# Optimization experiments

Measured on AMD Instinct MI355X. Metric: run time of the kernel, lower is better.

The kernel has to match this reference:

```python
import jax, jax.numpy as jnp
import numpy as np

H = 16        # num heads
ALPHA = 1.3   # entmax alpha
N_ITER = 50   # bisection iterations
EPS = 1e-5    # layernorm eps


def entmax_bisect(x, alpha=ALPHA, n_iter=N_ITER):
    # x: (..., K). Bisection entmax along last axis (Peters et al. 2019).
    am1 = alpha - 1.0
    x = x - jnp.max(x, axis=-1, keepdims=True)
    m = jnp.max(x, axis=-1, keepdims=True)  # == 0 after shift
    lo, hi = m - 10.0, m + 10.0
    def step(carry, _):
        lo, hi = carry
        mid = 0.5 * (lo + hi)
        p = jnp.maximum(am1 * x - mid, 0.0) ** (1.0 / am1)
        gt = jnp.sum(p, axis=-1, keepdims=True) > 1.0
        return (jnp.where(gt, mid, lo), jnp.where(gt, hi, mid)), None
    (lo, hi), _ = jax.lax.scan(jax.checkpoint(step), (lo, hi), None, length=n_iter)
    p = jnp.maximum(am1 * x - hi, 0.0) ** (1.0 / am1)
    return p / (jnp.sum(p, axis=-1, keepdims=True) + 1e-12)


def _heads(t, B, N, hd):
    return t.reshape(B, N, H, hd).transpose(0, 2, 1, 3)  # (B,H,N,hd)


def attn_branch(x, mask, wq, bq, wk, bk, wv, bv, wo, bo, use_entmax):
    B, N, D = x.shape
    hd = D // H
    q = _heads(x @ wq + bq, B, N, hd)
    k = _heads(x @ wk + bk, B, N, hd)
    v = _heads(x @ wv + bv, B, N, hd)
    s = jnp.einsum('bhqd,bhkd->bhqk', q, k) / float(np.sqrt(hd)) + mask
    if use_entmax:
        s = s - jnp.max(s, axis=-1, keepdims=True)
        a = entmax_bisect(s)
    else:
        a = jax.nn.softmax(s, axis=-1)
    o = jnp.einsum('bhqk,bhkd->bhqd', a, v).transpose(0, 2, 1, 3).reshape(B, N, D)
    return o @ wo + bo


def layer_norm(x, g, b):
    m = jnp.mean(x, axis=-1, keepdims=True)
    v = jnp.mean((x - m) ** 2, axis=-1, keepdims=True)
    return (x - m) * jax.lax.rsqrt(v + EPS) * g + b


def setup_inputs():
    B, N, D, F, FILM, NMODS = 4, 512, 2048, 8192, 64, 10000
    key = jax.random.key(0)
    ks = iter(jax.random.split(key, 64))
    rn = lambda *s: jax.random.normal(next(ks), s, dtype=jnp.float32)
    inp = dict(
        x=rn(B, N, D),
        attn_mask_intra=jnp.zeros((N, N), jnp.float32),
        attn_mask_inter=jnp.zeros((N, N), jnp.float32),
        mods=jax.random.randint(next(ks), (B, N), 0, 9999),
        film_emb=rn(NMODS, FILM) * 0.02,
        film_gw=rn(FILM, D) * 0.02, film_gb=jnp.zeros((D,), jnp.float32),
        film_bw=rn(FILM, D) * 0.02, film_bb=jnp.zeros((D,), jnp.float32),
        gate_alpha=jnp.zeros((2,), jnp.float32),
        ln1_g=jnp.ones((D,), jnp.float32), ln1_b=jnp.zeros((D,), jnp.float32),
        ln2_g=jnp.ones((D,), jnp.float32), ln2_b=jnp.zeros((D,), jnp.float32),
        ffn_w1=rn(D, F) * 0.02, ffn_b1=jnp.zeros((F,), jnp.float32),
        ffn_w2=rn(F, D) * 0.02, ffn_b2=jnp.zeros((D,), jnp.float32),
    )
    for tag in ('a', 'e'):
        for nm in ('q', 'k', 'v', 'o'):
            inp['w%s_%s' % (nm, tag)] = rn(D, D) * 0.02
            inp['b%s_%s' % (nm, tag)] = jnp.zeros((D,), jnp.float32)
    return inp


def reference(x, attn_mask_intra, attn_mask_inter, mods,
              film_emb, film_gw, film_gb, film_bw, film_bb,
              gate_alpha, ln1_g, ln1_b, ln2_g, ln2_b,
              ffn_w1, ffn_b1, ffn_w2, ffn_b2,
              wq_a, bq_a, wk_a, bk_a, wv_a, bv_a, wo_a, bo_a,
              wq_e, bq_e, wk_e, bk_e, wv_e, bv_e, wo_e, bo_e):
    # FiLM modulation on the intra-module branch input
    e = film_emb[jnp.clip(mods, 1, None)]                      # (B,N,FILM)
    y_intra = (1.0 + e @ film_gw + film_gb) * x + (e @ film_bw + film_bb)
    z_intra = attn_branch(y_intra, attn_mask_intra, wq_a, bq_a, wk_a, bk_a,
                          wv_a, bv_a, wo_a, bo_a, use_entmax=False)
    z_inter = attn_branch(x, attn_mask_inter, wq_e, bq_e, wk_e, bk_e,
                          wv_e, bv_e, wo_e, bo_e, use_entmax=True)
    w = jax.nn.softmax(gate_alpha)                              # global gate
    z = w[0] * z_intra + w[1] * z_inter
    h = layer_norm(x + z, ln1_g, ln1_b)                         # Post-LN
    y = jax.nn.relu(h @ ffn_w1 + ffn_b1) @ ffn_w2 + ffn_b2
    return layer_norm(h + y, ln2_g, ln2_b)
```

## Files before the change

### kernel.cpp

```cpp
#include <hip/hip_runtime.h>
#include <hip/hip_bf16.h>

typedef float f32x4 __attribute__((ext_vector_type(4)));
typedef short bf16x8 __attribute__((ext_vector_type(8)));
typedef unsigned short u16;

#define SEQ    512
#define DIM    2048
#define NHEAD  16
#define HDIM   128
#define BATCH  4
#define BTOK   2048
#define FFDIM  8192
#define DSZ    ((long)BTOK*DIM)
#define QKVN   (3*DIM)
#define QKVSZ  ((long)BTOK*QKVN)
#define ISS    0.08838834764831845f

__device__ __forceinline__ u16 f2bf(float f){
  union{float fv;unsigned u;}c;c.fv=f;
  unsigned r=c.u+0x7FFFu+((c.u>>16)&1u); return (u16)(r>>16);
}
__device__ __forceinline__ float bf2f(u16 v){
  union{unsigned u;float f;}c;c.u=((unsigned)v)<<16;return c.f;
}
__device__ __forceinline__ float pow103(float t){
  return __builtin_amdgcn_exp2f(__builtin_amdgcn_logf(t)*(10.0f/3.0f));
}

#define GLD16(g,l) __builtin_amdgcn_global_load_lds( \
    (const __attribute__((address_space(1))) unsigned int*)(g), \
    (__attribute__((address_space(3))) unsigned int*)(l), 16, 0, 0)

#define MF(a,b,c) __builtin_amdgcn_mfma_f32_16x16x32_bf16(a,b,c,0,0,0)
#define VMW(n) do{ asm volatile("s_waitcnt vmcnt(" #n ")" ::: "memory"); \
                   __builtin_amdgcn_sched_barrier(0); }while(0)
#define LGKM0() do{ asm volatile("s_waitcnt lgkmcnt(0)" ::: "memory"); \
                    __builtin_amdgcn_sched_barrier(0); }while(0)
#define BARR() do{ asm volatile("" ::: "memory"); __builtin_amdgcn_s_barrier(); \
                   asm volatile("" ::: "memory"); }while(0)

__global__ __launch_bounds__(256, 2)
void gemm4w(const u16* __restrict__ A, int lda, long sAo, long sAi,
            const u16* __restrict__ B, int ldb, long sBo, long sBi,
            u16* __restrict__ C, int ldc, long sCo,
            const float* __restrict__ bias, long sbias,
            int K, int hdiv, int relu)
{
  __shared__ __align__(16) u16 sm[36864];
  char* smb = (char*)sm;

  int gx = gridDim.x, gy = gridDim.y;
  int nwg = gx*gy*gridDim.z;
  int flat = (blockIdx.z*gy + blockIdx.y)*gx + blockIdx.x;
  int cpx = nwg >> 3; flat = (flat & 7)*cpx + (flat >> 3);
  int by = flat % gy; int tq = flat / gy; int bx = tq % gx; int bz = tq / gx;

  int zo = bz / hdiv, zi = bz - zo*hdiv;
  const u16* Ab = A + (long)zo*sAo + (long)zi*sAi;
  const u16* Bb = B + (long)zo*sBo + (long)zi*sBi;
  int m0 = by*128, n0 = bx*256;

  int tid = threadIdx.x, lane = tid & 63, w = tid >> 6;
  int lr = lane & 15, lg = lane >> 4;
  int rl = lane >> 2, cbyte = (lane & 3)*16;

  int sRA[2], sCA[2];
  #pragma unroll
  for (int q = 0; q < 2; q++) {
    int r = (2*w+q)*16 + rl;
    sRA[q] = r ^ ((r>>2)&1);
    sCA[q] = (cbyte ^ ((((r>>2)^r)&1)<<4) ^ (((r>>1)&1)<<5)) >> 1;
  }
  int sRB[4], sCB[4];
  #pragma unroll
  for (int q = 0; q < 4; q++) {
    int r = (4*w+q)*16 + rl;
    sRB[q] = r ^ ((r>>2)&1);
    sCB[q] = (cbyte ^ ((((r>>2)^r)&1)<<4) ^ (((r>>1)&1)<<5)) >> 1;
  }

  int aoff = (lr*64 + lg*16) ^ ((lane&7)<<4);
  int boff = w*4096 + ((lr*64 + lg*16) ^ ((lane&7)<<4));

  f32x4 acc[8][4] = {};
  int NT = K >> 5;

  auto STG = [&](int buf, int kt) {
    int kcol = kt*32;
    char* base = smb + buf*24576;
    #pragma unroll
    for (int q = 0; q < 2; q++)
      GLD16(Ab + (long)(m0 + sRA[q])*lda + kcol + sCA[q], base + (2*w+q)*1024);
    #pragma unroll
    for (int q = 0; q < 4; q++)
      GLD16(Bb + (long)(n0 + sRB[q])*ldb + kcol + sCB[q], base + 8192 + (4*w+q)*1024);
  };

  STG(0,0);
  if (NT > 1) STG(1,1);

  int buf = 0;
  for (int t = 0; t < NT; t++) {
    char* Ax = smb + buf*24576;
    char* Bx = Ax + 8192;

    if (t+2 < NT) {
      int nb = buf + 2; if (nb >= 3) nb -= 3;
      STG(nb, t+2);
      VMW(12);
    } else if (t+1 < NT) { VMW(6); }
    else                 { VMW(0); }
    BARR();

    bf16x8 af[8], bv[4];
    #pragma unroll
    for (int i = 0; i < 8; i++) af[i] = *(const bf16x8*)(Ax + aoff + i*1024);
    #pragma unroll
    for (int j = 0; j < 4; j++) bv[j] = *(const bf16x8*)(Bx + boff + j*1024);
    LGKM0();
    __builtin_amdgcn_s_setprio(1);
    #pragma unroll
    for (int i = 0; i < 8; i++) {
      acc[i][0] = MF(af[i], bv[0], acc[i][0]);
      acc[i][1] = MF(af[i], bv[1], acc[i][1]);
      acc[i][2] = MF(af[i], bv[2], acc[i][2]);
      acc[i][3] = MF(af[i], bv[3], acc[i][3]);
    }
    __builtin_amdgcn_s_setprio(0);
    BARR();
    buf++; if (buf == 3) buf = 0;
  }

  u16* Cb = C + (long)bz*sCo;
  #pragma unroll
  for (int j = 0; j < 4; j++) {
    int col = n0 + w*64 + j*16 + lr;
    float bv2 = bias ? bias[zo*sbias + col] : 0.0f;
    #pragma unroll
    for (int i = 0; i < 8; i++) {
      #pragma unroll
      for (int e = 0; e < 4; e++) {
        int row = m0 + i*16 + lg*4 + e;
        float v = acc[i][j][e] + bv2;
        if (relu) v = fmaxf(v, 0.0f);
        Cb[(long)row*ldc + col] = f2bf(v);
      }
    }
  }
}

__global__ __launch_bounds__(256, 3)
void gemm4(const u16* __restrict__ A, int lda, long sAo, long sAi,
           const u16* __restrict__ B, int ldb, long sBo, long sBi,
           void* __restrict__ C, int ldc, long sCo, long sCi, int outbf,
           const float* __restrict__ bias, long sbias,
           int K, int hdiv, int relu)
{
  __shared__ __align__(16) u16 sm[24576];
  char* smb = (char*)sm;

  int gx = gridDim.x, gy = gridDim.y;
  int nwg = gx*gy*gridDim.z;
  int flat = (blockIdx.z*gy + blockIdx.y)*gx + blockIdx.x;
  int cpx = nwg >> 3; flat = (flat & 7)*cpx + (flat >> 3);
  int by = flat % gy; int tq = flat / gy; int bx = tq % gx; int bz = tq / gx;

  int zo = bz / hdiv, zi = bz - zo*hdiv;
  const u16* Ab = A + (long)zo*sAo + (long)zi*sAi;
  const u16* Bb = B + (long)zo*sBo + (long)zi*sBi;
  int m0 = by*128, n0 = bx*128;

  int tid = threadIdx.x, lane = tid & 63, w = tid >> 6;
  int wrow = (w>>1)*64, wn = (w&1)*64;
  int lr = lane & 15, lg = lane >> 4;

  int stR[2], stC[2], ldsch[2];
  #pragma unroll
  for (int q = 0; q < 2; q++) {
    int chunk = q*4 + w;
    int r = chunk*16 + (lane>>2);
    int c = (lane&3)*16;
    int Rz = r ^ ((r>>2)&1);
    int Cz = c ^ ((((r>>2)^r)&1)<<4) ^ (((r>>1)&1)<<5);
    stR[q] = Rz; stC[q] = Cz>>1;
    ldsch[q] = chunk*1024;
  }

  int aoff = ((wrow + lr)*64 + lg*16) ^ ((lane&7)<<4);
  int boff = ((wn  + lr)*64 + lg*16) ^ ((lane&7)<<4);

  f32x4 acc[4][4] = {};
  int NT = K >> 5;

  auto STG = [&](int buf, int op, int kt) {
    const u16* gp = op ? Bb : Ab;
    int ld   = op ? ldb : lda;
    int base = op ? n0 : m0;
    int kcol = kt*32;
    #pragma unroll
    for (int q = 0; q < 2; q++) {
      const u16* src = gp + (long)(base + stR[q])*ld + kcol + stC[q];
      char* dst = smb + buf*16384 + op*8192 + ldsch[q];
      GLD16(src, dst);
    }
  };

  STG(0,0,0); STG(0,1,0);
  if (NT > 1) { STG(1,0,1); STG(1,1,1); }

  int buf = 0;
  for (int t = 0; t < NT; t++) {
    char* Ax = smb + buf*16384;
    char* Bx = smb + buf*16384 + 8192;

    if (t+2 < NT) {
      int nb = buf + 2; if (nb >= 3) nb -= 3;
      STG(nb,0,t+2); STG(nb,1,t+2);
      VMW(8);
    } else if (t+1 < NT) { VMW(4); }
    else                 { VMW(0); }
    BARR();

    bf16x8 af[4], bv[4];
    #pragma unroll
    for (int i = 0; i < 4; i++) af[i] = *(const bf16x8*)(Ax + aoff + i*1024);
    #pragma unroll
    for (int j = 0; j < 4; j++) bv[j] = *(const bf16x8*)(Bx + boff + j*1024);
    LGKM0();
    __builtin_amdgcn_s_setprio(1);
    #pragma unroll
    for (int i = 0; i < 4; i++) {
      acc[i][0] = MF(af[i], bv[0], acc[i][0]);
      acc[i][1] = MF(af[i], bv[1], acc[i][1]);
      acc[i][2] = MF(af[i], bv[2], acc[i][2]);
      acc[i][3] = MF(af[i], bv[3], acc[i][3]);
    }
    __builtin_amdgcn_s_setprio(0);
    BARR();
    buf++; if (buf == 3) buf = 0;
  }

  long coff = (long)zo*sCo + (long)zi*sCi;
  if (outbf) {
    u16* Cb = (u16*)C + coff;
    #pragma unroll
    for (int j = 0; j < 4; j++) {
      int col = n0 + wn + j*16 + lr;
      float bv2 = bias ? bias[zo*sbias + col] : 0.0f;
      #pragma unroll
      for (int i = 0; i < 4; i++) {
        #pragma unroll
        for (int e = 0; e < 4; e++) {
          int row = m0 + wrow + i*16 + lg*4 + e;
          float v = acc[i][j][e] + bv2;
          if (relu) v = fmaxf(v, 0.0f);
          Cb[(long)row*ldc + col] = f2bf(v);
        }
      }
    }
  } else {
    float* Cb = (float*)C + coff;
    #pragma unroll
    for (int j = 0; j < 4; j++) {
      int col = n0 + wn + j*16 + lr;
      #pragma unroll
      for (int i = 0; i < 4; i++) {
        #pragma unroll
        for (int e = 0; e < 4; e++) {
          int row = m0 + wrow + i*16 + lg*4 + e;
          Cb[(long)row*ldc + col] = acc[i][j][e];
        }
      }
    }
  }
}

__global__ __launch_bounds__(256, 2)
void qkprobs_both(const u16* __restrict__ QKVp,
                  const float* __restrict__ maskI, const float* __restrict__ maskE,
                  u16* __restrict__ Pall)
{
  __shared__ __align__(16) u16 sm[40960];
  char* smb = (char*)sm;

  int m0 = blockIdx.x*64;
  int z2 = blockIdx.y;
  int br = z2 >> 6, z = z2 & 63;
  int b  = z >> 4, h = z & 15;
  const float* maskp = br ? maskE : maskI;
  const u16* Qb = QKVp + (long)br*QKVSZ + (long)b*SEQ*QKVN + h*HDIM;
  const u16* Kb = Qb + DIM;
  u16* P = Pall + (long)br*64*SEQ*SEQ;

  int tid = threadIdx.x, lane = tid & 63, w = tid >> 6;
  int lr = lane & 15, lg = lane >> 4;
  int wn = w*128;

  int rl = lane >> 2;
  int cb = (lane & 3)*16;

  int aoff = (lr*64 + lg*16) ^ ((lane&7)<<4);
  int boff = ((wn + lr)*64 + lg*16) ^ ((lane&7)<<4);

  auto stgA = [&](int kt) {
    int r = w*16 + rl;
    int Rz = r ^ ((r>>2)&1);
    int Cz = cb ^ ((((r>>2)^r)&1)<<4) ^ (((r>>1)&1)<<5);
    GLD16(Qb + (long)(m0+Rz)*QKVN + kt*32 + (Cz>>1), smb + kt*4096 + w*1024);
  };
  auto stgB = [&](int buf, int kt) {
    #pragma unroll
    for (int q = 0; q < 8; q++) {
      int chunk = q*4 + w;
      int r = chunk*16 + rl;
      int Rz = r ^ ((r>>2)&1);
      int Cz = cb ^ ((((r>>2)^r)&1)<<4) ^ (((r>>1)&1)<<5);
      GLD16(Kb + (long)Rz*QKVN + kt*32 + (Cz>>1),
            smb + 16384 + buf*32768 + chunk*1024);
    }
  };

  f32x4 acc[4][8] = {};

  stgA(0); stgA(1); stgA(2); stgA(3);
  stgB(0,0);

  #pragma unroll
  for (int kt = 0; kt < 4; kt++) {
    if (kt < 3) { stgB((kt+1)&1, kt+1); VMW(8); } else { VMW(0); }
    BARR();
    char* Bx = smb + 16384 + (kt&1)*32768;
    bf16x8 af[4], bv[8];
    #pragma unroll
    for (int i = 0; i < 4; i++) af[i] = *(const bf16x8*)(smb + kt*4096 + aoff + i*1024);
    #pragma unroll
    for (int j = 0; j < 8; j++) bv[j] = *(const bf16x8*)(Bx + boff + j*1024);
    LGKM0();
    __builtin_amdgcn_s_setprio(1);
    #pragma unroll
    for (int i = 0; i < 4; i++)
      #pragma unroll
      for (int j = 0; j < 8; j++)
        acc[i][j] = MF(af[i], bv[j], acc[i][j]);
    __builtin_amdgcn_s_setprio(0);
    BARR();
  }

  float* redA = (float*)smb;
  float* redB = (float*)(smb + 1024);

  float rmax[16];
  #pragma unroll
  for (int s = 0; s < 16; s++) rmax[s] = -3.4e38f;
  #pragma unroll
  for (int i = 0; i < 4; i++) {
    #pragma unroll
    for (int e = 0; e < 4; e++) {
      int row = i*16 + lg*4 + e;
      const float* mp = maskp + (long)(m0+row)*SEQ + wn + lr;
      #pragma unroll
      for (int j = 0; j < 8; j++) {
        float v = acc[i][j][e]*ISS + mp[j*16];
        acc[i][j][e] = v;
        rmax[i*4+e] = fmaxf(rmax[i*4+e], v);
      }
    }
  }
  #pragma unroll
  for (int s = 0; s < 16; s++)
    #pragma unroll
    for (int o = 1; o < 16; o <<= 1) rmax[s] = fmaxf(rmax[s], __shfl_xor(rmax[s], o));
  if (lr == 0) {
    #pragma unroll
    for (int i = 0; i < 4; i++)
      #pragma unroll
      for (int e = 0; e < 4; e++) redA[w*64 + i*16 + lg*4 + e] = rmax[i*4+e];
  }
  BARR();
  #pragma unroll
  for (int i = 0; i < 4; i++)
    #pragma unroll
    for (int e = 0; e < 4; e++) {
      int row = i*16 + lg*4 + e;
      rmax[i*4+e] = fmaxf(fmaxf(redA[row], redA[64+row]),
                          fmaxf(redA[128+row], redA[192+row]));
    }
  BARR();

  float inv[16];

  if (br) {
    #pragma unroll
    for (int i = 0; i < 4; i++)
      #pragma unroll
      for (int j = 0; j < 8; j++)
        #pragma unroll
        for (int e = 0; e < 4; e++)
          acc[i][j][e] = (acc[i][j][e] - rmax[i*4+e])*0.3f;

    float lo[16], hi[16], tau[16];
    #pragma unroll
    for (int s = 0; s < 16; s++) { lo[s] = -1.0f; hi[s] = 0.0f; }

    #pragma unroll 1
    for (int it = 0; it < 5; it++) {
      float ps[16];
      #pragma unroll
      for (int s = 0; s < 16; s++) ps[s] = 0.0f;
      #pragma unroll
      for (int i = 0; i < 4; i++)
        #pragma unroll
        for (int e = 0; e < 4; e++) {
          float mid = 0.5f*(lo[i*4+e] + hi[i*4+e]);
          #pragma unroll
          for (int j = 0; j < 8; j++) {
            float t = acc[i][j][e] - mid;
            if (t > 0.0f) ps[i*4+e] += pow103(t);
          }
        }
      #pragma unroll
      for (int s = 0; s < 16; s++)
        #pragma unroll
        for (int o = 1; o < 16; o <<= 1) ps[s] += __shfl_xor(ps[s], o);
      if (lr == 0) {
        #pragma unroll
        for (int i = 0; i < 4; i++)
          #pragma unroll
          for (int e = 0; e < 4; e++) redA[w*64 + i*16 + lg*4 + e] = ps[i*4+e];
      }
      BARR();
      #pragma unroll
      for (int i = 0; i < 4; i++)
        #pragma unroll
        for (int e = 0; e < 4; e++) {
          int row = i*16 + lg*4 + e, s = i*4+e;
          float tot = redA[row] + redA[64+row] + redA[128+row] + redA[192+row];
          float mid = 0.5f*(lo[s] + hi[s]);
          bool gt = tot > 1.0f;
          lo[s] = gt ? mid : lo[s];
          hi[s] = gt ? hi[s] : mid;
        }
      BARR();
    }
    #pragma unroll
    for (int s = 0; s < 16; s++) tau[s] = 0.5f*(lo[s] + hi[s]);

    #pragma unroll 1
    for (int it = 0; it < 5; it++) {
      float ps[16], pd[16];
      #pragma unroll
      for (int s = 0; s < 16; s++) { ps[s] = 0.0f; pd[s] = 0.0f; }
      #pragma unroll
      for (int i = 0; i < 4; i++)
        #pragma unroll
        for (int e = 0; e < 4; e++) {
          float tv = tau[i*4+e];
          #pragma unroll
          for (int j = 0; j < 8; j++) {
            float t = acc[i][j][e] - tv;
            if (t > 0.0f) {
              float w7 = __builtin_amdgcn_exp2f(__builtin_amdgcn_logf(t)*(7.0f/3.0f));
              pd[i*4+e] += w7; ps[i*4+e] += w7*t;
            }
          }
        }
      #pragma unroll
      for (int s = 0; s < 16; s++)
        #pragma unroll
        for (int o = 1; o < 16; o <<= 1) {
          ps[s] += __shfl_xor(ps[s], o);
          pd[s] += __shfl_xor(pd[s], o);
        }
      if (lr == 0) {
        #pragma unroll
        for (int i = 0; i < 4; i++)
          #pragma unroll
          for (int e = 0; e < 4; e++) {
            redA[w*64 + i*16 + lg*4 + e] = ps[i*4+e];
            redB[w*64 + i*16 + lg*4 + e] = pd[i*4+e];
          }
      }
      BARR();
      #pragma unroll
      for (int i = 0; i < 4; i++)
        #pragma unroll
        for (int e = 0; e < 4; e++) {
          int row = i*16 + lg*4 + e, s = i*4+e;
          float st = redA[row] + redA[64+row] + redA[128+row] + redA[192+row];
          float dt = redB[row] + redB[64+row] + redB[128+row] + redB[192+row];
          bool gt = st > 1.0f;
          lo[s] = gt ? tau[s] : lo[s];
          hi[s] = gt ? hi[s] : tau[s];
          float tn = tau[s] + (st - 1.0f) / ((10.0f/3.0f)*dt + 1e-30f);
          tau[s] = (tn > lo[s] && tn < hi[s]) ? tn : 0.5f*(lo[s] + hi[s]);
        }
      BARR();
    }

    float ps[16];
    #pragma unroll
    for (int s = 0; s < 16; s++) ps[s] = 0.0f;
    #pragma unroll
    for (int i = 0; i < 4; i++)
      #pragma unroll
      for (int e = 0; e < 4; e++) {
        float tv = tau[i*4+e];
        #pragma unroll
        for (int j = 0; j < 8; j++) {
          float t = acc[i][j][e] - tv;
          float p = (t > 0.0f) ? pow103(t) : 0.0f;
          acc[i][j][e] = p;
          ps[i*4+e] += p;
        }
      }
    #pragma unroll
    for (int s = 0; s < 16; s++)
      #pragma unroll
      for (int o = 1; o < 16; o <<= 1) ps[s] += __shfl_xor(ps[s], o);
    if (lr == 0) {
      #pragma unroll
      for (int i = 0; i < 4; i++)
        #pragma unroll
        for (int e = 0; e < 4; e++) redA[w*64 + i*16 + lg*4 + e] = ps[i*4+e];
    }
    BARR();
    #pragma unroll
    for (int i = 0; i < 4; i++)
      #pragma unroll
      for (int e = 0; e < 4; e++) {
        int row = i*16 + lg*4 + e;
        inv[i*4+e] = 1.0f/(redA[row] + redA[64+row] + redA[128+row] + redA[192+row] + 1e-12f);
      }
  } else {
    float ps[16];
    #pragma unroll
    for (int s = 0; s < 16; s++) ps[s] = 0.0f;
    #pragma unroll
    for (int i = 0; i < 4; i++)
      #pragma unroll
      for (int e = 0; e < 4; e++) {
        float mx = rmax[i*4+e];
        #pragma unroll
        for (int j = 0; j < 8; j++) {
          float p = __expf(acc[i][j][e] - mx);
          acc[i][j][e] = p;
          ps[i*4+e] += p;
        }
      }
    #pragma unroll
    for (int s = 0; s < 16; s++)
      #pragma unroll
      for (int o = 1; o < 16; o <<= 1) ps[s] += __shfl_xor(ps[s], o);
    if (lr == 0) {
      #pragma unroll
      for (int i = 0; i < 4; i++)
        #pragma unroll
        for (int e = 0; e < 4; e++) redA[w*64 + i*16 + lg*4 + e] = ps[i*4+e];
    }
    BARR();
    #pragma unroll
    for (int i = 0; i < 4; i++)
      #pragma unroll
      for (int e = 0; e < 4; e++) {
        int row = i*16 + lg*4 + e;
        inv[i*4+e] = 1.0f/(redA[row] + redA[64+row] + redA[128+row] + redA[192+row]);
      }
  }

  u16* Pb = P + ((long)z*SEQ + m0)*SEQ;
  #pragma unroll
  for (int i = 0; i < 4; i++)
    #pragma unroll
    for (int e = 0; e < 4; e++) {
      int row = i*16 + lg*4 + e;
      u16* pr = Pb + (long)row*SEQ + wn + lr;
      #pragma unroll
      for (int j = 0; j < 8; j++)
        pr[j*16] = f2bf(acc[i][j][e]*inv[i*4+e]);
    }
}

__global__ __launch_bounds__(256)
void redk(const float* __restrict__ Pp, int nk, const float* __restrict__ bias,
          u16* __restrict__ out)
{
  long i = ((long)blockIdx.x*256 + threadIdx.x)*8;
  long z = i >> 22;
  int  n = (int)(i & 2047);
  float v[8] = {};
  for (int k = 0; k < nk; k++) {
    const float* s = Pp + (z*nk + k)*DSZ + (i & (DSZ-1));
    f32x4 aa = *(const f32x4*)s, bb = *(const f32x4*)(s+4);
    v[0]+=aa.x; v[1]+=aa.y; v[2]+=aa.z; v[3]+=aa.w;
    v[4]+=bb.x; v[5]+=bb.y; v[6]+=bb.z; v[7]+=bb.w;
  }
  f32x4 b0 = *(const f32x4*)&bias[z*2048 + n], b1 = *(const f32x4*)&bias[z*2048 + n + 4];
  float bv[8] = {b0.x,b0.y,b0.z,b0.w,b1.x,b1.y,b1.z,b1.w};
  u16 w[8] __attribute__((aligned(16)));
  #pragma unroll
  for (int j = 0; j < 8; j++) w[j] = f2bf(v[j] + bv[j]);
  *(bf16x8*)&out[i] = *(bf16x8*)w;
}

template<int BN_, int WM_, int WN_>
__global__ __launch_bounds__(256)
void gemm_lds(const u16* __restrict__ A, int lda, long sAo, long sAi,
              const u16* __restrict__ B, int ldb, long sBo, long sBi,
              void* __restrict__ C, int ldc, long sCo, long sCi, int outbf,
              const float* __restrict__ bias, long sbias,
              float alpha, int K, int hdiv, int relu)
{
  constexpr int BM_ = 128;
  constexpr int MI = BM_/WM_/16;
  constexpr int NJ = BN_/WN_/16;
  __shared__ __align__(16) u16 As[BM_*32];
  __shared__ __align__(16) u16 Bs[BN_*32];

  int z = blockIdx.z, zo = z/hdiv, zi = z - zo*hdiv;
  const u16* Ab = A + zo*sAo + zi*sAi;
  const u16* Bb = B + zo*sBo + zi*sBi;

  int m0 = blockIdx.y*BM_, n0 = blockIdx.x*BN_;
  int tid = threadIdx.x, lane = tid & 63, wid = tid >> 6;
  int wrow = (wid/WN_)*(BM_/WM_), wcol = (wid%WN_)*(BN_/WN_);
  int lr = lane & 15, lg = lane >> 4;
  int srow = lane >> 2, skc = (lane & 3)*8;

  f32x4 acc[MI][NJ] = {};

  for (int k0 = 0; k0 < K; k0 += 32) {
    #pragma unroll
    for (int e = 0; e < BM_/64; e++) {
      int c = wid*(BM_/64) + e, row = c*16 + srow;
      GLD16(Ab + (long)(m0 + row)*lda + k0 + skc, &As[c*512]);
    }
    #pragma unroll
    for (int e = 0; e < BN_/64; e++) {
      int c = wid*(BN_/64) + e, row = c*16 + srow;
      GLD16(Bb + (long)(n0 + row)*ldb + k0 + skc, &Bs[c*512]);
    }
    __syncthreads();
    bf16x8 af[MI], bfv[NJ];
    #pragma unroll
    for (int i = 0; i < MI; i++)
      af[i] = *(const bf16x8*)&As[(wrow + i*16 + lr)*32 + lg*8];
    #pragma unroll
    for (int j = 0; j < NJ; j++)
      bfv[j] = *(const bf16x8*)&Bs[(wcol + j*16 + lr)*32 + lg*8];
    #pragma unroll
    for (int i = 0; i < MI; i++)
      #pragma unroll
      for (int j = 0; j < NJ; j++)
        acc[i][j] = MF(af[i], bfv[j], acc[i][j]);
    __syncthreads();
  }

  long coff = (long)zo*sCo + (long)zi*sCi;
  #pragma unroll
  for (int j = 0; j < NJ; j++) {
    int col = n0 + wcol + j*16 + lr;
    float bv = bias ? bias[zo*sbias + col] : 0.0f;
    #pragma unroll
    for (int i = 0; i < MI; i++) {
      #pragma unroll
      for (int e = 0; e < 4; e++) {
        int row = m0 + wrow + i*16 + lg*4 + e;
        float v = alpha*acc[i][j][e] + bv;
        if (relu)  v = fmaxf(v, 0.0f);
        long idx = coff + (long)row*ldc + col;
        if (outbf) ((u16*)C)[idx] = f2bf(v);
        else       ((float*)C)[idx] = v;
      }
    }
  }
}

struct P6 { const float* p[6]; };

__global__ __launch_bounds__(256)
void wtrans6(P6 srcs, int ldw, u16* __restrict__ Wt, long dstStride, int ldt)
{
  __shared__ u16 t[64][72];
  const float* W = srcs.p[blockIdx.z];
  u16* Wd = Wt + (long)blockIdx.z*dstStride;
  int tid = threadIdx.x, r = tid >> 2, c0 = (tid & 3)*16;
  long gr = (long)blockIdx.y*64 + r, gc = (long)blockIdx.x*64 + c0;
  #pragma unroll
  for (int u = 0; u < 16; u += 4) {
    f32x4 v = *(const f32x4*)&W[gr*ldw + gc + u];
    t[r][c0+u+0]=f2bf(v.x); t[r][c0+u+1]=f2bf(v.y);
    t[r][c0+u+2]=f2bf(v.z); t[r][c0+u+3]=f2bf(v.w);
  }
  __syncthreads();
  u16 o[16] __attribute__((aligned(16)));
  #pragma unroll
  for (int u = 0; u < 16; u++) o[u] = t[c0+u][r];
  u16* dst = &Wd[(long)(blockIdx.x*64 + r)*ldt + blockIdx.y*64 + c0];
  *(bf16x8*)&dst[0] = *(bf16x8*)&o[0];
  *(bf16x8*)&dst[8] = *(bf16x8*)&o[8];
}

__global__ __launch_bounds__(256)
void wtrans(const float* __restrict__ W, int ldw, u16* __restrict__ Wt, int ldt)
{
  __shared__ u16 t[64][72];
  int tid = threadIdx.x, r = tid >> 2, c0 = (tid & 3)*16;
  long gr = (long)blockIdx.y*64 + r, gc = (long)blockIdx.x*64 + c0;
  #pragma unroll
  for (int u = 0; u < 16; u += 4) {
    f32x4 v = *(const f32x4*)&W[gr*ldw + gc + u];
    t[r][c0+u+0]=f2bf(v.x); t[r][c0+u+1]=f2bf(v.y);
    t[r][c0+u+2]=f2bf(v.z); t[r][c0+u+3]=f2bf(v.w);
  }
  __syncthreads();
  u16 o[16] __attribute__((aligned(16)));
  #pragma unroll
  for (int u = 0; u < 16; u++) o[u] = t[c0+u][r];
  u16* dst = &Wt[(long)(blockIdx.x*64 + r)*ldt + blockIdx.y*64 + c0];
  *(bf16x8*)&dst[0] = *(bf16x8*)&o[0];
  *(bf16x8*)&dst[8] = *(bf16x8*)&o[8];
}

__global__ __launch_bounds__(256)
void vtrans_both(const u16* __restrict__ QKVp, u16* __restrict__ Vt)
{
  __shared__ u16 t[64][72];
  int z = blockIdx.z;
  int br = z >> 6, zz = z & 63, b = zz >> 4, h = zz & 15;
  const u16* src = QKVp + (long)br*QKVSZ + (long)b*SEQ*QKVN + h*HDIM + 2*DIM;
  u16* dst = Vt + (long)z*HDIM*SEQ;
  int tid = threadIdx.x, r = tid >> 2, c0 = (tid & 3)*16;
  int tok0 = blockIdx.x*64, d0 = blockIdx.y*64;
  #pragma unroll
  for (int u = 0; u < 16; u += 8) {
    bf16x8 v = *(const bf16x8*)&src[(long)(tok0+r)*QKVN + d0 + c0 + u];
    #pragma unroll
    for (int e = 0; e < 8; e++) t[r][c0+u+e] = (u16)v[e];
  }
  __syncthreads();
  u16 o[16] __attribute__((aligned(16)));
  #pragma unroll
  for (int u = 0; u < 16; u++) o[u] = t[c0+u][r];
  *(bf16x8*)&dst[(long)(d0+r)*SEQ + tok0 + c0]     = *(bf16x8*)&o[0];
  *(bf16x8*)&dst[(long)(d0+r)*SEQ + tok0 + c0 + 8] = *(bf16x8*)&o[8];
}

__global__ __launch_bounds__(256)
void f32_to_bf16(const float* __restrict__ in, u16* __restrict__ o, long n8)
{
  long i = (long)blockIdx.x*256 + threadIdx.x;
  if (i >= n8) return; i *= 8;
  f32x4 a = *(const f32x4*)&in[i], b = *(const f32x4*)&in[i+4];
  u16 w[8] __attribute__((aligned(16)));
  w[0]=f2bf(a.x);w[1]=f2bf(a.y);w[2]=f2bf(a.z);w[3]=f2bf(a.w);
  w[4]=f2bf(b.x);w[5]=f2bf(b.y);w[6]=f2bf(b.z);w[7]=f2bf(b.w);
  *(bf16x8*)&o[i] = *(bf16x8*)w;
}

__global__ __launch_bounds__(256)
void egather(const int* __restrict__ mods, const float* __restrict__ emb, u16* __restrict__ E)
{
  int i = blockIdx.x*256 + threadIdx.x;
  int row = i >> 3, j0 = (i & 7)*8;
  int m = mods[row]; if (m < 1) m = 1;
  const float* s = &emb[(long)m*64 + j0];
  f32x4 a = *(const f32x4*)s, b = *(const f32x4*)(s+4);
  u16 w[8] __attribute__((aligned(16)));
  w[0]=f2bf(a.x);w[1]=f2bf(a.y);w[2]=f2bf(a.z);w[3]=f2bf(a.w);
  w[4]=f2bf(b.x);w[5]=f2bf(b.y);w[6]=f2bf(b.z);w[7]=f2bf(b.w);
  *(bf16x8*)&E[(long)row*64 + j0] = *(bf16x8*)w;
}

__global__ __launch_bounds__(256)
void film_apply(const float* __restrict__ x, const u16* __restrict__ G,
                const u16* __restrict__ B, u16* __restrict__ y)
{
  long i = ((long)blockIdx.x*256 + threadIdx.x)*8;
  f32x4 x0 = *(const f32x4*)&x[i], x1 = *(const f32x4*)&x[i+4];
  bf16x8 g = *(const bf16x8*)&G[i], b = *(const bf16x8*)&B[i];
  float xv[8] = {x0.x,x0.y,x0.z,x0.w,x1.x,x1.y,x1.z,x1.w};
  u16 w[8] __attribute__((aligned(16)));
  #pragma unroll
  for (int e = 0; e < 8; e++)
    w[e] = f2bf((1.0f + bf2f((u16)g[e]))*xv[e] + bf2f((u16)b[e]));
  *(bf16x8*)&y[i] = *(bf16x8*)w;
}

__global__ __launch_bounds__(256)
void pack_bias(float* __restrict__ dst,
               const float* q_a, const float* k_a, const float* v_a,
               const float* q_e, const float* k_e, const float* v_e,
               const float* o_a, const float* o_e,
               const float* fg, const float* fb)
{
  int i = blockIdx.x*256 + threadIdx.x;
  if (i < 12288) {
    int br = i/6144, r = i - br*6144, sel = r >> 11, o = r & 2047;
    const float* s = br ? (sel==0?q_e:sel==1?k_e:v_e)
                        : (sel==0?q_a:sel==1?k_a:v_a);
    dst[i] = s[o];
  } else if (i < 16384) {
    int r = i - 12288; dst[i] = (r>>11) ? o_e[r&2047] : o_a[r&2047];
  } else {
    int r = i - 16384; dst[i] = (r>>11) ? fb[r&2047] : fg[r&2047];
  }
}

__global__ __launch_bounds__(256)
void ln_gate(const float* __restrict__ x, const u16* __restrict__ z0,
             const u16* __restrict__ z1, const float* __restrict__ ga,
             const float* __restrict__ g, const float* __restrict__ b,
             u16* __restrict__ h)
{
  __shared__ float red[8];
  long base = (long)blockIdx.x*DIM;
  int t8 = threadIdx.x*8, lane = threadIdx.x & 63, wid = threadIdx.x >> 6;
  float a0 = ga[0], a1 = ga[1];
  float mm = fmaxf(a0,a1), e0 = __expf(a0-mm), e1 = __expf(a1-mm);
  float w0 = e0/(e0+e1), w1 = e1/(e0+e1);
  f32x4 x0 = *(const f32x4*)&x[base+t8], x1 = *(const f32x4*)&x[base+t8+4];
  bf16x8 zi = *(const bf16x8*)&z0[base+t8], ze = *(const bf16x8*)&z1[base+t8];
  float xv[8] = {x0.x,x0.y,x0.z,x0.w,x1.x,x1.y,x1.z,x1.w};
  float v[8]; float s = 0.0f;
  #pragma unroll
  for (int j = 0; j < 8; j++) {
    v[j] = xv[j] + w0*bf2f((u16)zi[j]) + w1*bf2f((u16)ze[j]);
    s += v[j];
  }
  for (int o = 32; o; o >>= 1) s += __shfl_xor(s, o);
  if (lane == 0) red[wid] = s;
  __syncthreads();
  float mean = (red[0]+red[1]+red[2]+red[3])*(1.0f/DIM);
  float q = 0.0f;
  #pragma unroll
  for (int j = 0; j < 8; j++) { float d = v[j]-mean; q += d*d; }
  for (int o = 32; o; o >>= 1) q += __shfl_xor(q, o);
  if (lane == 0) red[4+wid] = q;
  __syncthreads();
  float inv = rsqrtf((red[4]+red[5]+red[6]+red[7])*(1.0f/DIM) + 1e-5f);
  f32x4 g0 = *(const f32x4*)&g[t8], g1 = *(const f32x4*)&g[t8+4];
  f32x4 b0 = *(const f32x4*)&b[t8], b1 = *(const f32x4*)&b[t8+4];
  float gv[8] = {g0.x,g0.y,g0.z,g0.w,g1.x,g1.y,g1.z,g1.w};
  float bv[8] = {b0.x,b0.y,b0.z,b0.w,b1.x,b1.y,b1.z,b1.w};
  u16 w[8] __attribute__((aligned(16)));
  #pragma unroll
  for (int j = 0; j < 8; j++) w[j] = f2bf((v[j]-mean)*inv*gv[j] + bv[j]);
  *(bf16x8*)&h[base+t8] = *(bf16x8*)w;
}

__global__ __launch_bounds__(256)
void ln_res(const u16* __restrict__ hin, const u16* __restrict__ y,
            const float* __restrict__ g, const float* __restrict__ b,
            float* __restrict__ out)
{
  __shared__ float red[8];
  long base = (long)blockIdx.x*DIM;
  int t8 = threadIdx.x*8, lane = threadIdx.x & 63, wid = threadIdx.x >> 6;
  bf16x8 hv = *(const bf16x8*)&hin[base+t8], yv = *(const bf16x8*)&y[base+t8];
  float v[8]; float s = 0.0f;
  #pragma unroll
  for (int j = 0; j < 8; j++) { v[j] = bf2f((u16)hv[j]) + bf2f((u16)yv[j]); s += v[j]; }
  for (int o = 32; o; o >>= 1) s += __shfl_xor(s, o);
  if (lane == 0) red[wid] = s;
  __syncthreads();
  float mean = (red[0]+red[1]+red[2]+red[3])*(1.0f/DIM);
  float q = 0.0f;
  #pragma unroll
  for (int j = 0; j < 8; j++) { float d = v[j]-mean; q += d*d; }
  for (int o = 32; o; o >>= 1) q += __shfl_xor(q, o);
  if (lane == 0) red[4+wid] = q;
  __syncthreads();
  float inv = rsqrtf((red[4]+red[5]+red[6]+red[7])*(1.0f/DIM) + 1e-5f);
  f32x4 g0 = *(const f32x4*)&g[t8], g1 = *(const f32x4*)&g[t8+4];
  f32x4 b0 = *(const f32x4*)&b[t8], b1 = *(const f32x4*)&b[t8+4];
  float gv[8] = {g0.x,g0.y,g0.z,g0.w,g1.x,g1.y,g1.z,g1.w};
  float bv[8] = {b0.x,b0.y,b0.z,b0.w,b1.x,b1.y,b1.z,b1.w};
  f32x4 o0, o1;
  #pragma unroll
  for (int j = 0; j < 4; j++) o0[j] = (v[j]-mean)*inv*gv[j] + bv[j];
  #pragma unroll
  for (int j = 0; j < 4; j++) o1[j] = (v[4+j]-mean)*inv*gv[4+j] + bv[4+j];
  *(f32x4*)&out[base+t8] = o0;
  *(f32x4*)&out[base+t8+4] = o1;
}

static void G4(hipStream_t st, const u16* A,int lda,long sAo,long sAi,
               const u16* B,int ldb,long sBo,long sBi,
               void* C,int ldc,long sCo,long sCi,int outbf,
               const float* bias,long sbias,int M,int N,int K,int batch,int hdiv,int relu)
{
  gemm4<<<dim3(N/128,M/128,batch),dim3(256),0,st>>>(
      A,lda,sAo,sAi,B,ldb,sBo,sBi,C,ldc,sCo,sCi,outbf,bias,sbias,K,hdiv,relu);
}
static void G4W(hipStream_t st, const u16* A,int lda,long sAo,long sAi,
                const u16* B,int ldb,long sBo,long sBi,
                u16* C,int ldc,long sCo,
                const float* bias,long sbias,int M,int N,int K,int batch,int hdiv,int relu)
{
  gemm4w<<<dim3(N/256,M/128,batch),dim3(256),0,st>>>(
      A,lda,sAo,sAi,B,ldb,sBo,sBi,C,ldc,sCo,bias,sbias,K,hdiv,relu);
}

extern "C" void kernel_launch(void* const* d_in, const int* in_sizes, int n_in,
                              void* d_out, int out_size, void* d_ws, size_t ws_size,
                              hipStream_t stream)
{
  const float* x          = (const float*)d_in[0];
  const float* mask_intra = (const float*)d_in[1];
  const float* mask_inter = (const float*)d_in[2];
  const int*   mods       = (const int*)  d_in[3];
  const float* film_emb   = (const float*)d_in[4];
  const float* film_gw    = (const float*)d_in[5];
  const float* film_gb    = (const float*)d_in[6];
  const float* film_bw    = (const float*)d_in[7];
  const float* film_bb    = (const float*)d_in[8];
  const float* gate_alpha = (const float*)d_in[9];
  const float* ln1_g = (const float*)d_in[10];
  const float* ln1_b = (const float*)d_in[11];
  const float* ln2_g = (const float*)d_in[12];
  const float* ln2_b = (const float*)d_in[13];
  const float* ffn_w1 = (const float*)d_in[14];
  const float* ffn_b1 = (const float*)d_in[15];
  const float* ffn_w2 = (const float*)d_in[16];
  const float* ffn_b2 = (const float*)d_in[17];
  const float* wq_a = (const float*)d_in[18]; const float* bq_a = (const float*)d_in[19];
  const float* wk_a = (const float*)d_in[20]; const float* bk_a = (const float*)d_in[21];
  const float* wv_a = (const float*)d_in[22]; const float* bv_a = (const float*)d_in[23];
  const float* wo_a = (const float*)d_in[24]; const float* bo_a = (const float*)d_in[25];
  const float* wq_e = (const float*)d_in[26]; const float* bq_e = (const float*)d_in[27];
  const float* wk_e = (const float*)d_in[28]; const float* bk_e = (const float*)d_in[29];
  const float* wv_e = (const float*)d_in[30]; const float* bv_e = (const float*)d_in[31];
  const float* wo_e = (const float*)d_in[32]; const float* bo_e = (const float*)d_in[33];

  char* ws = (char*)d_ws;
  u16*   ybf  = (u16*)(ws);
  u16*   xbf  = (u16*)(ws + (8L<<20));
  u16*   AO   = (u16*)(ws);
  u16*   QKV  = (u16*)(ws + (16L<<20));
  u16*   Gf   = QKV;
  u16*   Bfm  = QKV + DSZ;
  u16*   zbuf = (u16*)(ws + (16L<<20));
  u16*   hbf  = (u16*)(ws + (32L<<20));
  u16*   Wst  = (u16*)(ws + (64L<<20));
  u16*   Pall = (u16*)(ws + (96L<<20));
  u16*   mid  = (u16*)(ws + (96L<<20));
  float* Pf2  = (float*)(ws + (128L<<20));
  u16*   f2o  = (u16*)(ws + (16L<<20));
  u16*   Vt   = (u16*)(ws + (160L<<20));
  u16*   Ebuf = (u16*)(ws + (160L<<20));
  u16*   Wfm  = (u16*)(ws + (161L<<20));
  float* bpk  = (float*)(ws + (176L<<20));

  f32_to_bf16<<<2048,256,0,stream>>>(x, xbf, DSZ/8);
  egather<<<64,256,0,stream>>>(mods, film_emb, Ebuf);
  {
    P6 pf; pf.p[0]=film_gw; pf.p[1]=film_bw;
    pf.p[2]=film_gw; pf.p[3]=film_gw; pf.p[4]=film_gw; pf.p[5]=film_gw;
    wtrans6<<<dim3(32,1,2),256,0,stream>>>(pf, DIM, Wfm, (long)DIM*64, 64);
  }
  pack_bias<<<80,256,0,stream>>>(bpk, bq_a,bk_a,bv_a, bq_e,bk_e,bv_e, bo_a,bo_e, film_gb,film_bb);

  G4(stream, Ebuf,64,0,0, Wfm,64,(long)DIM*64,0, Gf,DIM,DSZ,0,1,
     bpk+16384,2048, BTOK,DIM,64, 2,1, 0);
  film_apply<<<2048,256,0,stream>>>(x, Gf, Bfm, ybf);

  {
    P6 pq; pq.p[0]=wq_a; pq.p[1]=wk_a; pq.p[2]=wv_a;
    pq.p[3]=wq_e; pq.p[4]=wk_e; pq.p[5]=wv_e;
    wtrans6<<<dim3(32,32,6),256,0,stream>>>(pq, DIM, Wst, (long)DIM*DIM, DIM);
  }
  G4W(stream, ybf,DIM,DSZ,0, Wst,DIM,(long)QKVN*DIM,0, QKV,QKVN,QKVSZ,
      bpk,QKVN, BTOK,QKVN,DIM, 2,1, 0);

  vtrans_both<<<dim3(8,2,128),256,0,stream>>>(QKV, Vt);
  qkprobs_both<<<dim3(8,128),dim3(256),0,stream>>>(QKV, mask_intra, mask_inter, Pall);
  G4(stream, Pall,SEQ,(long)16*SEQ*SEQ,(long)SEQ*SEQ,
     Vt,SEQ,(long)16*HDIM*SEQ,(long)HDIM*SEQ,
     AO,DIM,(long)SEQ*DIM,HDIM,1, nullptr,0,
     SEQ,HDIM,SEQ, 128,16, 0);

  {
    P6 po; po.p[0]=wo_a; po.p[1]=wo_e;
    po.p[2]=wo_a; po.p[3]=wo_a; po.p[4]=wo_a; po.p[5]=wo_a;
    wtrans6<<<dim3(32,32,2),256,0,stream>>>(po, DIM, Wst, (long)DIM*DIM, DIM);
  }
  G4(stream, AO,DIM,DSZ,0, Wst,DIM,(long)DIM*DIM,0, zbuf,DIM,DSZ,0,1,
     bpk+12288,DIM, BTOK,DIM,DIM, 2,1, 0);

  ln_gate<<<2048,256,0,stream>>>(x, zbuf, zbuf+DSZ, gate_alpha, ln1_g, ln1_b, hbf);

  wtrans<<<dim3(128,32),256,0,stream>>>(ffn_w1, FFDIM, Wst, DIM);
  G4W(stream, hbf,DIM,0,0, Wst,DIM,0,0, mid,FFDIM,0,
      ffn_b1,0, BTOK,FFDIM,DIM, 1,1, 1);
  wtrans<<<dim3(32,128),256,0,stream>>>(ffn_w2, DIM, Wst, FFDIM);
  G4(stream, mid,FFDIM,4096,0, Wst,FFDIM,4096,0, Pf2,DIM,DSZ,0,0,
     nullptr,0, BTOK,DIM,4096, 2,1, 0);
  redk<<<2048,256,0,stream>>>(Pf2, 2, ffn_b2, f2o);

  ln_res<<<2048,256,0,stream>>>(hbf, f2o, ln2_g, ln2_b, (float*)d_out);
}
```

Before: 621.7 us.

## Stage attention probabilities through LDS for coalesced stores and swap grid order

Result: slower. 638.7 us (+2.7%).

```diff
diff --git a/kernel.cpp b/kernel.cpp
--- a/kernel.cpp
+++ b/kernel.cpp
@@ -284,8 +284,8 @@
   __shared__ __align__(16) u16 sm[40960];
   char* smb = (char*)sm;
 
-  int m0 = blockIdx.x*64;
-  int z2 = blockIdx.y;
+  int z2 = blockIdx.x;
+  int m0 = blockIdx.y*64;
   int br = z2 >> 6, z = z2 & 63;
   int b  = z >> 4, h = z & 15;
   const float* maskp = br ? maskE : maskI;
@@ -568,17 +568,28 @@
       }
   }
 
+  BARR();
+  #pragma unroll
+  for (int i = 0; i < 4; i++)
+    #pragma unroll
+    for (int e = 0; e < 4; e++) {
+      int r = i*16 + lg*4 + e;
+      float sc = inv[i*4+e];
+      #pragma unroll
+      for (int j = 0; j < 8; j++) {
+        int cbyt = (wn + j*16 + lr)*2;
+        *(u16*)(smb + r*1024 + (cbyt ^ ((r&7)<<4))) = f2bf(acc[i][j][e]*sc);
+      }
+    }
+  BARR();
   u16* Pb = P + ((long)z*SEQ + m0)*SEQ;
   #pragma unroll
-  for (int i = 0; i < 4; i++)
-    #pragma unroll
-    for (int e = 0; e < 4; e++) {
-      int row = i*16 + lg*4 + e;
-      u16* pr = Pb + (long)row*SEQ + wn + lr;
-      #pragma unroll
-      for (int j = 0; j < 8; j++)
-        pr[j*16] = f2bf(acc[i][j][e]*inv[i*4+e]);
-    }
+  for (int chunk = 0; chunk < 16; chunk++) {
+    int p = chunk*4096 + tid*16;
+    int row = p >> 10, cb2 = p & 1023;
+    bf16x8 v = *(const bf16x8*)(smb + row*1024 + (cb2 ^ ((row&7)<<4)));
+    *(bf16x8*)((char*)Pb + p) = v;
+  }
 }
 
 __global__ __launch_bounds__(256)
@@ -601,79 +612,6 @@
   #pragma unroll
   for (int j = 0; j < 8; j++) w[j] = f2bf(v[j] + bv[j]);
   *(bf16x8*)&out[i] = *(bf16x8*)w;
-}
-
-template<int BN_, int WM_, int WN_>
-__global__ __launch_bounds__(256)
-void gemm_lds(const u16* __restrict__ A, int lda, long sAo, long sAi,
-              const u16* __restrict__ B, int ldb, long sBo, long sBi,
-              void* __restrict__ C, int ldc, long sCo, long sCi, int outbf,
-              const float* __restrict__ bias, long sbias,
-              float alpha, int K, int hdiv, int relu)
-{
-  constexpr int BM_ = 128;
-  constexpr int MI = BM_/WM_/16;
-  constexpr int NJ = BN_/WN_/16;
-  __shared__ __align__(16) u16 As[BM_*32];
-  __shared__ __align__(16) u16 Bs[BN_*32];
-
-  int z = blockIdx.z, zo = z/hdiv, zi = z - zo*hdiv;
-  const u16* Ab = A + zo*sAo + zi*sAi;
-  const u16* Bb = B + zo*sBo + zi*sBi;
-
-  int m0 = blockIdx.y*BM_, n0 = blockIdx.x*BN_;
-  int tid = threadIdx.x, lane = tid & 63, wid = tid >> 6;
-  int wrow = (wid/WN_)*(BM_/WM_), wcol = (wid%WN_)*(BN_/WN_);
-  int lr = lane & 15, lg = lane >> 4;
-  int srow = lane >> 2, skc = (lane & 3)*8;
-
-  f32x4 acc[MI][NJ] = {};
-
-  for (int k0 = 0; k0 < K; k0 += 32) {
-    #pragma unroll
-    for (int e = 0; e < BM_/64; e++) {
-      int c = wid*(BM_/64) + e, row = c*16 + srow;
-      GLD16(Ab + (long)(m0 + row)*lda + k0 + skc, &As[c*512]);
-    }
-    #pragma unroll
-    for (int e = 0; e < BN_/64; e++) {
-      int c = wid*(BN_/64) + e, row = c*16 + srow;
-      GLD16(Bb + (long)(n0 + row)*ldb + k0 + skc, &Bs[c*512]);
-    }
-    __syncthreads();
-    bf16x8 af[MI], bfv[NJ];
-    #pragma unroll
-    for (int i = 0; i < MI; i++)
-      af[i] = *(const bf16x8*)&As[(wrow + i*16 + lr)*32 + lg*8];
-    #pragma unroll
-    for (int j = 0; j < NJ; j++)
-      bfv[j] = *(const bf16x8*)&Bs[(wcol + j*16 + lr)*32 + lg*8];
-    #pragma unroll
-    for (int i = 0; i < MI; i++)
-      #pragma unroll
-      for (int j = 0; j < NJ; j++)
-        acc[i][j] = MF(af[i], bfv[j], acc[i][j]);
-    __syncthreads();
-  }
-
-  long coff = (long)zo*sCo + (long)zi*sCi;
-  #pragma unroll
-  for (int j = 0; j < NJ; j++) {
-    int col = n0 + wcol + j*16 + lr;
-    float bv = bias ? bias[zo*sbias + col] : 0.0f;
-    #pragma unroll
-    for (int i = 0; i < MI; i++) {
-      #pragma unroll
-      for (int e = 0; e < 4; e++) {
-        int row = m0 + wrow + i*16 + lg*4 + e;
-        float v = alpha*acc[i][j][e] + bv;
-        if (relu)  v = fmaxf(v, 0.0f);
-        long idx = coff + (long)row*ldc + col;
-        if (outbf) ((u16*)C)[idx] = f2bf(v);
-        else       ((float*)C)[idx] = v;
-      }
-    }
-  }
 }
 
 struct P6 { const float* p[6]; };
@@ -974,7 +912,7 @@
       bpk,QKVN, BTOK,QKVN,DIM, 2,1, 0);
 
   vtrans_both<<<dim3(8,2,128),256,0,stream>>>(QKV, Vt);
-  qkprobs_both<<<dim3(8,128),dim3(256),0,stream>>>(QKV, mask_intra, mask_inter, Pall);
+  qkprobs_both<<<dim3(128,8),dim3(256),0,stream>>>(QKV, mask_intra, mask_inter, Pall);
   G4(stream, Pall,SEQ,(long)16*SEQ*SEQ,(long)SEQ*SEQ,
      Vt,SEQ,(long)16*HDIM*SEQ,(long)HDIM*SEQ,
      AO,DIM,(long)SEQ*DIM,HDIM,1, nullptr,0,
```
